# Optimization experiments

Hardware: AMD Instinct MI355X
Metric: run time of the kernel (lower is better)

Reference implementation:

```python
import jax, jax.numpy as jnp
import numpy as np

B, N, IN, LAT, HID = 64, 128, 5, 3, 64
ALPHA = 0.1
NEG_SLOPE = 0.2  # GATv2Conv default negative_slope


def _w(key, fan_in, shape):
    return jax.random.normal(key, shape, jnp.float32) * (1.0 / np.sqrt(fan_in))


def setup_inputs():
    key = jax.random.key(0)
    ks = iter(jax.random.split(key, 64))
    d = {}
    d["batch"] = jax.random.normal(next(ks), (B, N, IN), jnp.float32)
    d["enc_w1"] = _w(next(ks), IN, (IN, HID));   d["enc_b1"] = jnp.zeros((HID,), jnp.float32)
    d["enc_w2"] = _w(next(ks), HID, (HID, HID)); d["enc_b2"] = jnp.zeros((HID,), jnp.float32)
    d["enc_w3"] = _w(next(ks), HID, (HID, LAT)); d["enc_b3"] = jnp.zeros((LAT,), jnp.float32)
    for i, cin in zip((1, 2, 3, 4), (1, HID, HID, HID)):
        d[f"g{i}_wl"] = _w(next(ks), cin, (cin, HID)); d[f"g{i}_bl"] = jnp.zeros((HID,), jnp.float32)
        d[f"g{i}_wr"] = _w(next(ks), cin, (cin, HID)); d[f"g{i}_br"] = jnp.zeros((HID,), jnp.float32)
        d[f"g{i}_att"] = _w(next(ks), HID, (HID,));    d[f"g{i}_b"] = jnp.zeros((HID,), jnp.float32)
    d["lab_w"] = _w(next(ks), HID, (HID, 4)); d["lab_b"] = jnp.zeros((4,), jnp.float32)
    d["val_w"] = _w(next(ks), HID, (HID, 1)); d["val_b"] = jnp.zeros((1,), jnp.float32)
    d["skip_w"] = _w(next(ks), LAT, (LAT, HID)); d["skip_b"] = jnp.zeros((HID,), jnp.float32)
    return d


def _gabriel_adj(p):
    """Gabriel graph adjacency, p: [N, LAT] -> bool [N, N] (symmetric, no diag).
    Edge (i,j) survives iff no witness k with |p_k - mid_ij|^2 < |p_i - p_j|^2 / 4."""
    n = p.shape[0]
    mid = 0.5 * (p[:, None, :] + p[None, :, :])                      # [n,n,d]
    r2 = 0.25 * jnp.sum((p[:, None, :] - p[None, :, :]) ** 2, -1)    # [n,n]
    pk2 = jnp.sum(p * p, -1)                                         # [n]
    m2 = jnp.sum(mid * mid, -1)                                      # [n,n]
    # d2[k,i,j] = |p_k - mid_ij|^2 via expansion (avoids [n,n,n,d] tensor)
    d2 = pk2[:, None, None] - 2.0 * jnp.einsum('kd,ijd->kij', p, mid) + m2[None]
    idx = jnp.arange(n)
    not_ij = (idx[:, None, None] != idx[None, :, None]) & (idx[:, None, None] != idx[None, None, :])
    blocked = jnp.any((d2 < r2[None]) & not_ij, axis=0)              # [n,n]
    return (~blocked) & (idx[:, None] != idx[None, :])


def _gatv2(x, adj, wl, bl, wr, br, att, b):
    """Dense single-head GATv2 (PyG GATv2Conv semantics, self-loops already in adj).
    x: [B,N,Cin], adj: bool [B,N,N] (adj[b,i,j] => edge j->i)."""
    hl = x @ wl + bl   # source transform (lin_l)
    hr = x @ wr + br   # target transform (lin_r)
    e = jax.nn.leaky_relu(hr[:, :, None, :] + hl[:, None, :, :], NEG_SLOPE)  # [B,i,j,H]
    s = jnp.einsum('bijh,h->bij', e, att)
    s = jnp.where(adj, s, -1e30)
    a = jax.nn.softmax(s, axis=-1)                                   # softmax over neighbors j of i
    return jnp.einsum('bij,bjh->bih', a, hl) + b


def reference(batch, enc_w1, enc_b1, enc_w2, enc_b2, enc_w3, enc_b3,
              g1_wl, g1_bl, g1_wr, g1_br, g1_att, g1_b,
              g2_wl, g2_bl, g2_wr, g2_br, g2_att, g2_b,
              g3_wl, g3_bl, g3_wr, g3_br, g3_att, g3_b,
              g4_wl, g4_bl, g4_wr, g4_br, g4_att, g4_b,
              lab_w, lab_b, val_w, val_b, skip_w, skip_b):
    relu = jax.nn.relu
    h = relu(batch @ enc_w1 + enc_b1)
    h = relu(h @ enc_w2 + enc_b2)
    latent = h @ enc_w3 + enc_b3                                     # [B,N,3]

    adj = jax.vmap(_gabriel_adj)(jax.lax.stop_gradient(latent))      # bool [B,N,N]
    adj_sl = adj | jnp.eye(N, dtype=bool)                            # add_self_loops=True

    x0 = latent[..., 2:3]                                            # node feature = 3rd latent coord
    x1 = relu(_gatv2(x0, adj_sl, g1_wl, g1_bl, g1_wr, g1_br, g1_att, g1_b))
    x2 = relu(_gatv2(x1, adj_sl, g2_wl, g2_bl, g2_wr, g2_br, g2_att, g2_b))
    skip = latent @ skip_w + skip_b
    x3 = relu(_gatv2(x2, adj_sl, g3_wl, g3_bl, g3_wr, g3_br, g3_att, g3_b) + ALPHA * skip)
    logits = x3 @ lab_w + lab_b                                      # [B,N,4]
    x4 = relu(_gatv2(x2, adj_sl, g4_wl, g4_bl, g4_wr, g4_br, g4_att, g4_b) + ALPHA * skip)
    values = x4 @ val_w + val_b                                      # [B,N,1]

    # dense edge attributes: pairwise latent distances masked by the Gabriel adjacency
    d2p = jnp.sum((latent[:, :, None, :] - latent[:, None, :, :]) ** 2, -1)
    edge_dist = jnp.sqrt(jnp.where(adj, d2p, 1.0)) * adj

    return (batch[:, :, :4], batch[:, :, 4:5], logits, values, latent, adj, edge_dist)
```

## Files before the change

### kernel.cpp

```cpp
#include <hip/hip_runtime.h>

#define BB 64
#define NN 128
#define INF_ 5
#define LATD 3
#define HIDD 64

__device__ __forceinline__ float bflo(unsigned u) { return __uint_as_float(u << 16); }
__device__ __forceinline__ float bfhi(unsigned u) { return __uint_as_float(u & 0xffff0000u); }
__device__ __forceinline__ unsigned bfpack(float a, float b) {
    unsigned ua = __float_as_uint(a), ub = __float_as_uint(b);
    unsigned ra = (ua + 0x7fffu + ((ua >> 16) & 1u)) >> 16;
    unsigned rb = (ub + 0x7fffu + ((ub >> 16) & 1u)) >> 16;
    return ra | (rb << 16);
}

__global__ __launch_bounds__(256) void enc_kernel(
    const float* __restrict__ batch,
    const float* __restrict__ w1, const float* __restrict__ b1,
    const float* __restrict__ w2, const float* __restrict__ b2,
    const float* __restrict__ w3, const float* __restrict__ b3,
    double* __restrict__ aos,
    float* __restrict__ o0, float* __restrict__ o1, float* __restrict__ o4,
    float* __restrict__ o5)
{
    const int b = blockIdx.x;
    const int n0 = blockIdx.y * 32;
    const int tid = threadIdx.x;
    const int w = tid >> 6, lane = tid & 63;

    {
        const int blk = blockIdx.x * 4 + blockIdx.y;
        float4* z = (float4*)o5 + (size_t)blk * 2048;
        float4 zero = make_float4(0.f, 0.f, 0.f, 0.f);
        for (int q = tid; q < 2048; q += 256) z[q] = zero;
    }

    __shared__ double xs[32][6];
    __shared__ double w1s[INF_][HIDD];
    __shared__ float  w2s[HIDD * HIDD];
    __shared__ double w3s[HIDD][LATD];
    __shared__ double b1s[HIDD], b2s[HIDD], b3s[LATD];

    for (int idx = tid; idx < 32 * INF_; idx += 256) {
        int n = idx / INF_, c = idx % INF_;
        float v = batch[((size_t)b * NN + n0 + n) * INF_ + c];
        xs[n][c] = (double)v;
        if (c < 4) o0[((size_t)b * NN + n0 + n) * 4 + c] = v;
        else       o1[(size_t)b * NN + n0 + n] = v;
    }
    for (int idx = tid; idx < INF_ * HIDD; idx += 256)
        w1s[idx / HIDD][idx % HIDD] = (double)w1[idx];
    for (int idx = tid; idx < HIDD * HIDD; idx += 256)
        w2s[idx] = w2[idx];
    for (int idx = tid; idx < HIDD * LATD; idx += 256)
        w3s[idx / LATD][idx % LATD] = (double)w3[idx];
    if (tid < HIDD) {
        b1s[tid] = (double)b1[tid];
        b2s[tid] = (double)b2[tid];
    }
    if (tid < LATD) b3s[tid] = (double)b3[tid];
    __syncthreads();

    for (int r = 0; r < 8; ++r) {
        const int nl = w * 8 + r;
        const int n = n0 + nl;
        double h1v = b1s[lane];
        for (int k = 0; k < INF_; ++k) h1v += xs[nl][k] * w1s[k][lane];
        h1v = fmax(h1v, 0.0);
        double h2v = b2s[lane];
        for (int k = 0; k < HIDD; ++k) {
            double h1k = __shfl(h1v, k, 64);
            h2v += h1k * (double)w2s[k * HIDD + lane];
        }
        h2v = fmax(h2v, 0.0);
        double l0 = h2v * w3s[lane][0];
        double l1 = h2v * w3s[lane][1];
        double l2 = h2v * w3s[lane][2];
        for (int o = 32; o >= 1; o >>= 1) {
            l0 += __shfl_xor(l0, o, 64);
            l1 += __shfl_xor(l1, o, 64);
            l2 += __shfl_xor(l2, o, 64);
        }
        l0 += b3s[0]; l1 += b3s[1]; l2 += b3s[2];
        if (lane == 0) {
            double* A = aos + ((size_t)b * NN + n) * 4;
            A[0] = l0; A[1] = l1; A[2] = l2;
            A[3] = l0 * l0 + l1 * l1 + l2 * l2;
        }
        if (lane < LATD) {
            double lv = (lane == 0) ? l0 : ((lane == 1) ? l1 : l2);
            o4[((size_t)b * NN + n) * LATD + lane] = (float)lv;
        }
    }
}

__global__ __launch_bounds__(256) void gabriel_kernel(
    const double* __restrict__ aos,
    float* __restrict__ o5, float* __restrict__ o6)
{
    const int b = blockIdx.y;
    const int w = threadIdx.x >> 6, lane = threadIdx.x & 63;
    const int u = blockIdx.x * 4 + w;
    const int v = u >> 1, par = u & 1;

    __shared__ double4 Ps[NN];
    const double2* src = (const double2*)(aos + (size_t)b * NN * 4);
    double2* dst = (double2*)Ps;
    for (int idx = threadIdx.x; idx < NN * 2; idx += 256) dst[idx] = src[idx];
    __syncthreads();

    const double4 A  = Ps[lane];
    const double4 Bq = Ps[lane + 64];

    for (int half = 0; half < 2; ++half) {
        const int i = (half == 0) ? v : 126 - v;
        if (half == 1 && i == v) break;
        const int jstart = (half == 0) ? (v + 1) : (127 - v);
        const int j0 = jstart + ((jstart ^ par) & 1);
        const double4 pi = Ps[i];
        const double aix = A.x - pi.x,  aiy = A.y - pi.y,  aiz = A.z - pi.z;
        const double bix = Bq.x - pi.x, biy = Bq.y - pi.y, biz = Bq.z - pi.z;
        const bool mA = (lane != i), mB = (lane + 64 != i);
        for (int j = j0; j < NN; j += 2) {
            double4 pj = Ps[j];
            double ajx = A.x - pj.x,  ajy = A.y - pj.y,  ajz = A.z - pj.z;
            double bjx = Bq.x - pj.x, bjy = Bq.y - pj.y, bjz = Bq.z - pj.z;
            double dA = aix * ajx + aiy * ajy + aiz * ajz;
            double dB = bix * bjx + biy * bjy + biz * bjz;
            bool tA = (dA < 0.0) && mA && (lane != j);
            bool tB = (dB < 0.0) && mB && (lane + 64 != j);
            if (!__any(tA || tB)) {
                if (lane == 0) {
                    double dx = pi.x - pj.x, dy = pi.y - pj.y, dz = pi.z - pj.z;
                    float d = (float)sqrt(dx * dx + dy * dy + dz * dz);
                    size_t ij = ((size_t)b * NN + i) * NN + j;
                    size_t ji = ((size_t)b * NN + j) * NN + i;
                    o5[ij] = 1.0f; o5[ji] = 1.0f;
                    o6[ij] = d;    o6[ji] = d;
                }
            }
        }
    }
}

template <int CIN>
__device__ __forceinline__ void lin_body(
    int b, int n0, const float* __restrict__ xin, const float* __restrict__ latf,
    const float* __restrict__ wl, const float* __restrict__ bl,
    const float* __restrict__ wr, const float* __restrict__ br,
    unsigned* __restrict__ hlp, unsigned* __restrict__ hrp,
    float4* xs4, int tid)
{
    float* xsh = (float*)xs4;
    if constexpr (CIN == 64) {
        const float4* src = (const float4*)(xin + ((size_t)b * NN + n0) * HIDD);
        for (int idx = tid; idx < 32 * 16; idx += 256) xs4[idx] = src[idx];
    } else {
        if (tid < 32) xsh[tid] = latf[((size_t)b * NN + n0 + tid) * LATD + 2];
    }
    __syncthreads();

    const int w = tid >> 6, lane = tid & 63;
    float wc[CIN];
    #pragma unroll
    for (int k = 0; k < CIN; ++k) wc[k] = wl[k * HIDD + lane];
    float bv = bl[lane];
    for (int m = 0; m < 8; ++m) {
        int nl = w * 8 + m;
        float acc = bv;
        if constexpr (CIN == 64) {
            #pragma unroll
            for (int t = 0; t < 16; ++t) {
                float4 q = xs4[nl * 16 + t];
                acc = fmaf(q.x, wc[4 * t + 0], acc);
                acc = fmaf(q.y, wc[4 * t + 1], acc);
                acc = fmaf(q.z, wc[4 * t + 2], acc);
                acc = fmaf(q.w, wc[4 * t + 3], acc);
            }
        } else acc = fmaf(xsh[nl], wc[0], acc);
        float partner = __shfl_xor(acc, 1, 64);
        if ((lane & 1) == 0)
            hlp[((size_t)b * NN + n0 + nl) * 32 + (lane >> 1)] = bfpack(acc, partner);
    }
    #pragma unroll
    for (int k = 0; k < CIN; ++k) wc[k] = wr[k * HIDD + lane];
    bv = br[lane];
    for (int m = 0; m < 8; ++m) {
        int nl = w * 8 + m;
        float acc = bv;
        if constexpr (CIN == 64) {
            #pragma unroll
            for (int t = 0; t < 16; ++t) {
                float4 q = xs4[nl * 16 + t];
                acc = fmaf(q.x, wc[4 * t + 0], acc);
                acc = fmaf(q.y, wc[4 * t + 1], acc);
                acc = fmaf(q.z, wc[4 * t + 2], acc);
                acc = fmaf(q.w, wc[4 * t + 3], acc);
            }
        } else acc = fmaf(xsh[nl], wc[0], acc);
        float partner = __shfl_xor(acc, 1, 64);
        if ((lane & 1) == 0)
            hrp[((size_t)b * NN + n0 + nl) * 32 + (lane >> 1)] = bfpack(acc, partner);
    }
}

template <int CIN>
__global__ __launch_bounds__(256) void lin_kernel(
    const float* __restrict__ xin, const float* __restrict__ latf,
    const float* __restrict__ wl, const float* __restrict__ bl,
    const float* __restrict__ wr, const float* __restrict__ br,
    unsigned* __restrict__ hlp, unsigned* __restrict__ hrp)
{
    __shared__ float4 xs4[(CIN == 64) ? 32 * 16 : 8];
    lin_body<CIN>(blockIdx.x >> 2, (blockIdx.x & 3) << 5, xin, latf,
                  wl, bl, wr, br, hlp, hrp, xs4, threadIdx.x);
}

__global__ __launch_bounds__(256) void lin34_kernel(
    const float* __restrict__ xin,
    const float* __restrict__ wl3, const float* __restrict__ bl3,
    const float* __restrict__ wr3, const float* __restrict__ br3,
    const float* __restrict__ wl4, const float* __restrict__ bl4,
    const float* __restrict__ wr4, const float* __restrict__ br4,
    unsigned* __restrict__ hl3p, unsigned* __restrict__ hr3p,
    unsigned* __restrict__ hl4p, unsigned* __restrict__ hr4p)
{
    __shared__ float4 xs4[32 * 16];
    const int b = blockIdx.x >> 2, n0 = (blockIdx.x & 3) << 5;
    if (blockIdx.y == 0)
        lin_body<64>(b, n0, xin, nullptr, wl3, bl3, wr3, br3, hl3p, hr3p, xs4, threadIdx.x);
    else
        lin_body<64>(b, n0, xin, nullptr, wl4, bl4, wr4, br4, hl4p, hr4p, xs4, threadIdx.x);
}

struct AttnS {
    float  hls[NN * 66];
    float2 as2[4][NN];
    float2 hr2[8][32];
    float2 att2[32];
};

template <int C>
__device__ __forceinline__ void attn_v3(
    int b, int i0, int tid, AttnS& s,
    const unsigned* __restrict__ hlp, const unsigned* __restrict__ hrp,
    const float* __restrict__ att, const float* __restrict__ bias,
    const float* __restrict__ adjf, const float* __restrict__ latf,
    const float* __restrict__ skw, const float* __restrict__ skb,
    float* __restrict__ xout,
    const float* __restrict__ head_w, const float* __restrict__ head_b,
    float* __restrict__ head_out)
{
    const int w = tid >> 6, lane = tid & 63;

    {
        const unsigned* src = hlp + (size_t)b * NN * 32;
        for (int idx = tid; idx < NN * 32; idx += 256) {
            int j = idx >> 5, c = idx & 31;
            unsigned u = src[idx];
            *(float2*)&s.hls[j * 66 + 2 * c] = make_float2(bflo(u), bfhi(u));
        }
        unsigned u = hrp[((size_t)b * NN + i0) * 32 + tid];
        ((float2*)s.hr2)[tid] = make_float2(bflo(u), bfhi(u));
        if (tid < 32) s.att2[tid] = make_float2(att[2 * tid], att[2 * tid + 1]);
    }
    float bsv = bias[lane];
    float sw0 = 0.f, sw1 = 0.f, sw2 = 0.f, sbv = 0.f;
    if (skw != nullptr) {
        sw0 = skw[lane]; sw1 = skw[64 + lane]; sw2 = skw[128 + lane];
        sbv = skb[lane];
    }
    __syncthreads();

    const int il0 = w * 2, il1 = il0 + 1;
    const int i_0 = i0 + il0, i_1 = i0 + il1;

    float s00 = 0.f, s01 = 0.f, s10 = 0.f, s11 = 0.f;
    {
        const float* hl0 = &s.hls[lane * 66];
        const float* hl1 = &s.hls[(lane + 64) * 66];
        #pragma unroll
        for (int c = 0; c < 32; ++c) {
            float2 av = s.att2[c];
            float2 r0 = s.hr2[il0][c];
            float2 r1 = s.hr2[il1][c];
            float2 g0 = *(const float2*)&hl0[2 * c];
            float2 g1 = *(const float2*)&hl1[2 * c];
            float e;
            e = r0.x + g0.x; e = fmaxf(e, 0.2f * e); s00 = fmaf(av.x, e, s00);
            e = r0.y + g0.y; e = fmaxf(e, 0.2f * e); s00 = fmaf(av.y, e, s00);
            e = r0.x + g1.x; e = fmaxf(e, 0.2f * e); s01 = fmaf(av.x, e, s01);
            e = r0.y + g1.y; e = fmaxf(e, 0.2f * e); s01 = fmaf(av.y, e, s01);
            e = r1.x + g0.x; e = fmaxf(e, 0.2f * e); s10 = fmaf(av.x, e, s10);
            e = r1.y + g0.y; e = fmaxf(e, 0.2f * e); s10 = fmaf(av.y, e, s10);
            e = r1.x + g1.x; e = fmaxf(e, 0.2f * e); s11 = fmaf(av.x, e, s11);
            e = r1.y + g1.y; e = fmaxf(e, 0.2f * e); s11 = fmaf(av.y, e, s11);
        }
    }
    {
        const float* ar0 = adjf + ((size_t)b * NN + i_0) * NN;
        const float* ar1 = adjf + ((size_t)b * NN + i_1) * NN;
        if (!((ar0[lane] != 0.f)      || (lane == i_0)))      s00 = -1e30f;
        if (!((ar0[lane + 64] != 0.f) || (lane + 64 == i_0))) s01 = -1e30f;
        if (!((ar1[lane] != 0.f)      || (lane == i_1)))      s10 = -1e30f;
        if (!((ar1[lane + 64] != 0.f) || (lane + 64 == i_1))) s11 = -1e30f;
    }
    float m0 = fmaxf(s00, s01), m1 = fmaxf(s10, s11);
    for (int o = 32; o >= 1; o >>= 1) {
        m0 = fmaxf(m0, __shfl_xor(m0, o, 64));
        m1 = fmaxf(m1, __shfl_xor(m1, o, 64));
    }
    float e00 = __expf(s00 - m0), e01 = __expf(s01 - m0);
    float e10 = __expf(s10 - m1), e11 = __expf(s11 - m1);
    float z0 = e00 + e01, z1 = e10 + e11;
    for (int o = 32; o >= 1; o >>= 1) {
        z0 += __shfl_xor(z0, o, 64);
        z1 += __shfl_xor(z1, o, 64);
    }
    float iv0 = 1.f / z0, iv1 = 1.f / z1;
    s.as2[w][lane]      = make_float2(e00 * iv0, e10 * iv1);
    s.as2[w][lane + 64] = make_float2(e01 * iv0, e11 * iv1);

    float o0a = 0.f, o1a = 0.f;
    for (int j = 0; j < NN; ++j) {
        float2 av = s.as2[w][j];
        float hv = s.hls[j * 66 + lane];
        o0a = fmaf(av.x, hv, o0a);
        o1a = fmaf(av.y, hv, o1a);
    }

    #pragma unroll
    for (int r = 0; r < 2; ++r) {
        const int i = (r == 0) ? i_0 : i_1;
        float out = ((r == 0) ? o0a : o1a) + bsv;
        if (skw != nullptr) {
            const float* lr = latf + ((size_t)b * NN + i) * LATD;
            float sk = sbv;
            sk = fmaf(lr[0], sw0, sk);
            sk = fmaf(lr[1], sw1, sk);
            sk = fmaf(lr[2], sw2, sk);
            out += 0.1f * sk;
        }
        out = fmaxf(out, 0.f);
        if constexpr (C == 0) {
            xout[((size_t)b * NN + i) * HIDD + lane] = out;
        } else {
            float hv[C > 0 ? C : 1];
            #pragma unroll
            for (int c = 0; c < C; ++c) {
                float vv = out * head_w[lane * C + c];
                for (int o = 32; o >= 1; o >>= 1) vv += __shfl_xor(vv, o, 64);
                hv[c] = vv + head_b[c];
            }
            if (lane == 0)
                for (int c = 0; c < C; ++c)
                    head_out[((size_t)b * NN + i) * C + c] = hv[c];
        }
    }
}

__global__ __launch_bounds__(256, 4) void attn12_kernel(
    const unsigned* __restrict__ hlp, const unsigned* __restrict__ hrp,
    const float* __restrict__ att, const float* __restrict__ bias,
    const float* __restrict__ adjf, float* __restrict__ xout)
{
    __shared__ AttnS s;
    attn_v3<0>(blockIdx.x >> 4, (blockIdx.x & 15) << 3, threadIdx.x, s,
               hlp, hrp, att, bias, adjf, nullptr, nullptr, nullptr,
               xout, nullptr, nullptr, nullptr);
}

__global__ __launch_bounds__(256, 4) void attn34_kernel(
    const unsigned* __restrict__ hl3p, const unsigned* __restrict__ hr3p,
    const unsigned* __restrict__ hl4p, const unsigned* __restrict__ hr4p,
    const float* __restrict__ att3, const float* __restrict__ b3,
    const float* __restrict__ att4, const float* __restrict__ b4,
    const float* __restrict__ adjf, const float* __restrict__ latf,
    const float* __restrict__ skw, const float* __restrict__ skb,
    const float* __restrict__ lab_w, const float* __restrict__ lab_b, float* __restrict__ o2,
    const float* __restrict__ val_w, const float* __restrict__ val_b, float* __restrict__ o3)
{
    __shared__ AttnS s;
    const int b = blockIdx.x >> 4, i0 = (blockIdx.x & 15) << 3;
    if (blockIdx.y == 0)
        attn_v3<4>(b, i0, threadIdx.x, s, hl3p, hr3p, att3, b3, adjf, latf,
                   skw, skb, nullptr, lab_w, lab_b, o2);
    else
        attn_v3<1>(b, i0, threadIdx.x, s, hl4p, hr4p, att4, b4, adjf, latf,
                   skw, skb, nullptr, val_w, val_b, o3);
}

extern "C" void kernel_launch(void* const* d_in, const int* in_sizes, int n_in,
                              void* d_out, int out_size, void* d_ws, size_t ws_size,
                              hipStream_t stream)
{
    const float* batch  = (const float*)d_in[0];
    const float* enc_w1 = (const float*)d_in[1];
    const float* enc_b1 = (const float*)d_in[2];
    const float* enc_w2 = (const float*)d_in[3];
    const float* enc_b2 = (const float*)d_in[4];
    const float* enc_w3 = (const float*)d_in[5];
    const float* enc_b3 = (const float*)d_in[6];
    const float* g_wl[4]  = {(const float*)d_in[7],  (const float*)d_in[13], (const float*)d_in[19], (const float*)d_in[25]};
    const float* g_bl[4]  = {(const float*)d_in[8],  (const float*)d_in[14], (const float*)d_in[20], (const float*)d_in[26]};
    const float* g_wr[4]  = {(const float*)d_in[9],  (const float*)d_in[15], (const float*)d_in[21], (const float*)d_in[27]};
    const float* g_br[4]  = {(const float*)d_in[10], (const float*)d_in[16], (const float*)d_in[22], (const float*)d_in[28]};
    const float* g_att[4] = {(const float*)d_in[11], (const float*)d_in[17], (const float*)d_in[23], (const float*)d_in[29]};
    const float* g_b[4]   = {(const float*)d_in[12], (const float*)d_in[18], (const float*)d_in[24], (const float*)d_in[30]};
    const float* lab_w = (const float*)d_in[31];
    const float* lab_b = (const float*)d_in[32];
    const float* val_w = (const float*)d_in[33];
    const float* val_b = (const float*)d_in[34];
    const float* skw   = (const float*)d_in[35];
    const float* skb   = (const float*)d_in[36];

    float* out = (float*)d_out;
    float* o0 = out;
    float* o1 = out + 32768;
    float* o2 = out + 40960;
    float* o3 = out + 73728;
    float* o4 = out + 81920;
    float* o5 = out + 106496;
    float* o6 = out + 1155072;

    char* p = (char*)d_ws;
    auto carve = [&](size_t bytes) { void* r = (void*)p; p += (bytes + 255) & ~(size_t)255; return r; };
    double*   aos  = (double*)  carve((size_t)BB * NN * 4 * 8);
    float*    xA   = (float*)   carve((size_t)BB * NN * HIDD * 4);
    float*    xB   = (float*)   carve((size_t)BB * NN * HIDD * 4);
    unsigned* hlp  = (unsigned*)carve((size_t)BB * NN * 32 * 4);
    unsigned* hrp  = (unsigned*)carve((size_t)BB * NN * 32 * 4);
    unsigned* hl3p = (unsigned*)carve((size_t)BB * NN * 32 * 4);
    unsigned* hr3p = (unsigned*)carve((size_t)BB * NN * 32 * 4);

    enc_kernel<<<dim3(BB, 4), 256, 0, stream>>>(batch, enc_w1, enc_b1, enc_w2, enc_b2,
                                                enc_w3, enc_b3, aos, o0, o1, o4, o5);
    gabriel_kernel<<<dim3(32, BB), 256, 0, stream>>>(aos, o5, o6);

    lin_kernel<1><<<BB * 4, 256, 0, stream>>>(nullptr, o4, g_wl[0], g_bl[0], g_wr[0], g_br[0], hlp, hrp);
    attn12_kernel<<<BB * 16, 256, 0, stream>>>(hlp, hrp, g_att[0], g_b[0], o5, xA);
    lin_kernel<64><<<BB * 4, 256, 0, stream>>>(xA, nullptr, g_wl[1], g_bl[1], g_wr[1], g_br[1], hlp, hrp);
    attn12_kernel<<<BB * 16, 256, 0, stream>>>(hlp, hrp, g_att[1], g_b[1], o5, xB);
    lin34_kernel<<<dim3(BB * 4, 2), 256, 0, stream>>>(xB,
        g_wl[2], g_bl[2], g_wr[2], g_br[2], g_wl[3], g_bl[3], g_wr[3], g_br[3],
        hl3p, hr3p, hlp, hrp);
    attn34_kernel<<<dim3(BB * 16, 2), 256, 0, stream>>>(hl3p, hr3p, hlp, hrp,
        g_att[2], g_b[2], g_att[3], g_b[3], o5, o4, skw, skb,
        lab_w, lab_b, o2, val_w, val_b, o3);
}
```

Before: 304.9 us.

## Fuse GATv2 linear projections into preceding attention kernels

Removes the separate lin kernels by computing the next layer's left/right projections at the end of each attention block, using the aggregated per-node outputs held in registers plus weight matrices staged in shared memory. Layer 1's rank-1 projection is computed inline at the start of the first attention kernel. This cuts three kernel launches and the fp32 xA/xB activation round trips through global memory. In exchange, every attention block reloads the full 64x64 weight matrices into LDS (four times in attnB), adds extra barriers, and performs a serial 64-step shuffle matvec.

```diff
diff --git a/kernel.cpp b/kernel.cpp
--- a/kernel.cpp
+++ b/kernel.cpp
@@ -144,96 +144,6 @@
     }
 }
 
-template <int CIN>
-__device__ __forceinline__ void lin_body(
-    int b, int n0, const float* __restrict__ xin, const float* __restrict__ latf,
-    const float* __restrict__ wl, const float* __restrict__ bl,
-    const float* __restrict__ wr, const float* __restrict__ br,
-    unsigned* __restrict__ hlp, unsigned* __restrict__ hrp,
-    float4* xs4, int tid)
-{
-    float* xsh = (float*)xs4;
-    if constexpr (CIN == 64) {
-        const float4* src = (const float4*)(xin + ((size_t)b * NN + n0) * HIDD);
-        for (int idx = tid; idx < 32 * 16; idx += 256) xs4[idx] = src[idx];
-    } else {
-        if (tid < 32) xsh[tid] = latf[((size_t)b * NN + n0 + tid) * LATD + 2];
-    }
-    __syncthreads();
-
-    const int w = tid >> 6, lane = tid & 63;
-    float wc[CIN];
-    #pragma unroll
-    for (int k = 0; k < CIN; ++k) wc[k] = wl[k * HIDD + lane];
-    float bv = bl[lane];
-    for (int m = 0; m < 8; ++m) {
-        int nl = w * 8 + m;
-        float acc = bv;
-        if constexpr (CIN == 64) {
-            #pragma unroll
-            for (int t = 0; t < 16; ++t) {
-                float4 q = xs4[nl * 16 + t];
-                acc = fmaf(q.x, wc[4 * t + 0], acc);
-                acc = fmaf(q.y, wc[4 * t + 1], acc);
-                acc = fmaf(q.z, wc[4 * t + 2], acc);
-                acc = fmaf(q.w, wc[4 * t + 3], acc);
-            }
-        } else acc = fmaf(xsh[nl], wc[0], acc);
-        float partner = __shfl_xor(acc, 1, 64);
-        if ((lane & 1) == 0)
-            hlp[((size_t)b * NN + n0 + nl) * 32 + (lane >> 1)] = bfpack(acc, partner);
-    }
-    #pragma unroll
-    for (int k = 0; k < CIN; ++k) wc[k] = wr[k * HIDD + lane];
-    bv = br[lane];
-    for (int m = 0; m < 8; ++m) {
-        int nl = w * 8 + m;
-        float acc = bv;
-        if constexpr (CIN == 64) {
-            #pragma unroll
-            for (int t = 0; t < 16; ++t) {
-                float4 q = xs4[nl * 16 + t];
-                acc = fmaf(q.x, wc[4 * t + 0], acc);
-                acc = fmaf(q.y, wc[4 * t + 1], acc);
-                acc = fmaf(q.z, wc[4 * t + 2], acc);
-                acc = fmaf(q.w, wc[4 * t + 3], acc);
-            }
-        } else acc = fmaf(xsh[nl], wc[0], acc);
-        float partner = __shfl_xor(acc, 1, 64);
-        if ((lane & 1) == 0)
-            hrp[((size_t)b * NN + n0 + nl) * 32 + (lane >> 1)] = bfpack(acc, partner);
-    }
-}
-
-template <int CIN>
-__global__ __launch_bounds__(256) void lin_kernel(
-    const float* __restrict__ xin, const float* __restrict__ latf,
-    const float* __restrict__ wl, const float* __restrict__ bl,
-    const float* __restrict__ wr, const float* __restrict__ br,
-    unsigned* __restrict__ hlp, unsigned* __restrict__ hrp)
-{
-    __shared__ float4 xs4[(CIN == 64) ? 32 * 16 : 8];
-    lin_body<CIN>(blockIdx.x >> 2, (blockIdx.x & 3) << 5, xin, latf,
-                  wl, bl, wr, br, hlp, hrp, xs4, threadIdx.x);
-}
-
-__global__ __launch_bounds__(256) void lin34_kernel(
-    const float* __restrict__ xin,
-    const float* __restrict__ wl3, const float* __restrict__ bl3,
-    const float* __restrict__ wr3, const float* __restrict__ br3,
-    const float* __restrict__ wl4, const float* __restrict__ bl4,
-    const float* __restrict__ wr4, const float* __restrict__ br4,
-    unsigned* __restrict__ hl3p, unsigned* __restrict__ hr3p,
-    unsigned* __restrict__ hl4p, unsigned* __restrict__ hr4p)
-{
-    __shared__ float4 xs4[32 * 16];
-    const int b = blockIdx.x >> 2, n0 = (blockIdx.x & 3) << 5;
-    if (blockIdx.y == 0)
-        lin_body<64>(b, n0, xin, nullptr, wl3, bl3, wr3, br3, hl3p, hr3p, xs4, threadIdx.x);
-    else
-        lin_body<64>(b, n0, xin, nullptr, wl4, bl4, wr4, br4, hl4p, hr4p, xs4, threadIdx.x);
-}
-
 struct AttnS {
     float  hls[NN * 66];
     float2 as2[4][NN];
@@ -241,41 +151,28 @@
     float2 att2[32];
 };
 
-template <int C>
-__device__ __forceinline__ void attn_v3(
-    int b, int i0, int tid, AttnS& s,
+__device__ __forceinline__ void attn_stage_packed(
+    AttnS& s, int tid, int b, int i0,
     const unsigned* __restrict__ hlp, const unsigned* __restrict__ hrp,
-    const float* __restrict__ att, const float* __restrict__ bias,
-    const float* __restrict__ adjf, const float* __restrict__ latf,
-    const float* __restrict__ skw, const float* __restrict__ skb,
-    float* __restrict__ xout,
-    const float* __restrict__ head_w, const float* __restrict__ head_b,
-    float* __restrict__ head_out)
-{
-    const int w = tid >> 6, lane = tid & 63;
-
-    {
-        const unsigned* src = hlp + (size_t)b * NN * 32;
-        for (int idx = tid; idx < NN * 32; idx += 256) {
-            int j = idx >> 5, c = idx & 31;
-            unsigned u = src[idx];
-            *(float2*)&s.hls[j * 66 + 2 * c] = make_float2(bflo(u), bfhi(u));
-        }
-        unsigned u = hrp[((size_t)b * NN + i0) * 32 + tid];
-        ((float2*)s.hr2)[tid] = make_float2(bflo(u), bfhi(u));
-        if (tid < 32) s.att2[tid] = make_float2(att[2 * tid], att[2 * tid + 1]);
-    }
-    float bsv = bias[lane];
-    float sw0 = 0.f, sw1 = 0.f, sw2 = 0.f, sbv = 0.f;
-    if (skw != nullptr) {
-        sw0 = skw[lane]; sw1 = skw[64 + lane]; sw2 = skw[128 + lane];
-        sbv = skb[lane];
-    }
-    __syncthreads();
-
+    const float* __restrict__ att)
+{
+    const unsigned* src = hlp + (size_t)b * NN * 32;
+    for (int idx = tid; idx < NN * 32; idx += 256) {
+        int j = idx >> 5, c = idx & 31;
+        unsigned u = src[idx];
+        *(float2*)&s.hls[j * 66 + 2 * c] = make_float2(bflo(u), bfhi(u));
+    }
+    unsigned u = hrp[((size_t)b * NN + i0) * 32 + tid];
+    ((float2*)s.hr2)[tid] = make_float2(bflo(u), bfhi(u));
+    if (tid < 32) s.att2[tid] = make_float2(att[2 * tid], att[2 * tid + 1]);
+}
+
+__device__ __forceinline__ void attn_phase(
+    AttnS& s, int b, int i0, int w, int lane,
+    const float* __restrict__ adjf, float& agg0, float& agg1)
+{
     const int il0 = w * 2, il1 = il0 + 1;
     const int i_0 = i0 + il0, i_1 = i0 + il1;
-
     float s00 = 0.f, s01 = 0.f, s10 = 0.f, s11 = 0.f;
     {
         const float* hl0 = &s.hls[lane * 66];
@@ -321,7 +218,6 @@
     float iv0 = 1.f / z0, iv1 = 1.f / z1;
     s.as2[w][lane]      = make_float2(e00 * iv0, e10 * iv1);
     s.as2[w][lane + 64] = make_float2(e01 * iv0, e11 * iv1);
-
     float o0a = 0.f, o1a = 0.f;
     for (int j = 0; j < NN; ++j) {
         float2 av = s.as2[w][j];
@@ -329,49 +225,148 @@
         o0a = fmaf(av.x, hv, o0a);
         o1a = fmaf(av.y, hv, o1a);
     }
+    agg0 = o0a; agg1 = o1a;
+}
+
+__device__ __forceinline__ void matvec_store(
+    AttnS& s, int tid, int w, int lane, float out0, float out1,
+    int b, int i0, const float* __restrict__ wmat, const float* __restrict__ bvec,
+    unsigned* __restrict__ outp)
+{
+    __syncthreads();
+    for (int idx = tid; idx < HIDD * HIDD; idx += 256) s.hls[idx] = wmat[idx];
+    __syncthreads();
+    float acc0 = bvec[lane], acc1 = acc0;
+    for (int h = 0; h < HIDD; ++h) {
+        float wv = s.hls[h * HIDD + lane];
+        acc0 = fmaf(__shfl(out0, h, 64), wv, acc0);
+        acc1 = fmaf(__shfl(out1, h, 64), wv, acc1);
+    }
+    float p0 = __shfl_xor(acc0, 1, 64);
+    float p1 = __shfl_xor(acc1, 1, 64);
+    if ((lane & 1) == 0) {
+        outp[((size_t)b * NN + i0 + w * 2 + 0) * 32 + (lane >> 1)] = bfpack(acc0, p0);
+        outp[((size_t)b * NN + i0 + w * 2 + 1) * 32 + (lane >> 1)] = bfpack(acc1, p1);
+    }
+}
+
+__global__ __launch_bounds__(256, 4) void attnA_kernel(
+    const float* __restrict__ latf,
+    const float* __restrict__ wl1, const float* __restrict__ bl1,
+    const float* __restrict__ wr1, const float* __restrict__ br1,
+    const float* __restrict__ att, const float* __restrict__ bias,
+    const float* __restrict__ adjf,
+    const float* __restrict__ wl2, const float* __restrict__ bl2,
+    const float* __restrict__ wr2, const float* __restrict__ br2,
+    unsigned* __restrict__ hl2p, unsigned* __restrict__ hr2p)
+{
+    __shared__ AttnS s;
+    const int bx = blockIdx.x;
+    const int b = bx >> 4, i0 = (bx & 15) << 3;
+    const int tid = threadIdx.x, w = tid >> 6, lane = tid & 63;
+
+    {
+        float wv = wl1[lane], bv = bl1[lane];
+        for (int m = 0; m < 32; ++m) {
+            int j = w + 4 * m;
+            float x0 = latf[((size_t)b * NN + j) * LATD + 2];
+            s.hls[j * 66 + lane] = fmaf(x0, wv, bv);
+        }
+    }
+    {
+        int il = tid >> 5, c = tid & 31;
+        float x0 = latf[((size_t)b * NN + i0 + il) * LATD + 2];
+        s.hr2[il][c] = make_float2(fmaf(x0, wr1[2 * c], br1[2 * c]),
+                                   fmaf(x0, wr1[2 * c + 1], br1[2 * c + 1]));
+    }
+    if (tid < 32) s.att2[tid] = make_float2(att[2 * tid], att[2 * tid + 1]);
+    float bsv = bias[lane];
+    __syncthreads();
+
+    float agg0, agg1;
+    attn_phase(s, b, i0, w, lane, adjf, agg0, agg1);
+    float out0 = fmaxf(agg0 + bsv, 0.f);
+    float out1 = fmaxf(agg1 + bsv, 0.f);
+
+    matvec_store(s, tid, w, lane, out0, out1, b, i0, wl2, bl2, hl2p);
+    matvec_store(s, tid, w, lane, out0, out1, b, i0, wr2, br2, hr2p);
+}
+
+__global__ __launch_bounds__(256, 4) void attnB_kernel(
+    const unsigned* __restrict__ hlp, const unsigned* __restrict__ hrp,
+    const float* __restrict__ att, const float* __restrict__ bias,
+    const float* __restrict__ adjf,
+    const float* __restrict__ wl3, const float* __restrict__ bl3,
+    const float* __restrict__ wr3, const float* __restrict__ br3,
+    const float* __restrict__ wl4, const float* __restrict__ bl4,
+    const float* __restrict__ wr4, const float* __restrict__ br4,
+    unsigned* __restrict__ hl3p, unsigned* __restrict__ hr3p,
+    unsigned* __restrict__ hl4p, unsigned* __restrict__ hr4p)
+{
+    __shared__ AttnS s;
+    const int bx = blockIdx.x;
+    const int b = bx >> 4, i0 = (bx & 15) << 3;
+    const int tid = threadIdx.x, w = tid >> 6, lane = tid & 63;
+
+    attn_stage_packed(s, tid, b, i0, hlp, hrp, att);
+    float bsv = bias[lane];
+    __syncthreads();
+
+    float agg0, agg1;
+    attn_phase(s, b, i0, w, lane, adjf, agg0, agg1);
+    float out0 = fmaxf(agg0 + bsv, 0.f);
+    float out1 = fmaxf(agg1 + bsv, 0.f);
+
+    matvec_store(s, tid, w, lane, out0, out1, b, i0, wl3, bl3, hl3p);
+    matvec_store(s, tid, w, lane, out0, out1, b, i0, wr3, br3, hr3p);
+    matvec_store(s, tid, w, lane, out0, out1, b, i0, wl4, bl4, hl4p);
+    matvec_store(s, tid, w, lane, out0, out1, b, i0, wr4, br4, hr4p);
+}
+
+template <int C>
+__device__ __forceinline__ void attn_head(
+    AttnS& s, int tid, int b, int i0,
+    const unsigned* __restrict__ hlp, const unsigned* __restrict__ hrp,
+    const float* __restrict__ att, const float* __restrict__ bias,
+    const float* __restrict__ adjf, const float* __restrict__ latf,
+    const float* __restrict__ skw, const float* __restrict__ skb,
+    const float* __restrict__ head_w, const float* __restrict__ head_b,
+    float* __restrict__ head_out)
+{
+    const int w = tid >> 6, lane = tid & 63;
+    attn_stage_packed(s, tid, b, i0, hlp, hrp, att);
+    float bsv = bias[lane];
+    float sw0 = skw[lane], sw1 = skw[64 + lane], sw2 = skw[128 + lane];
+    float sbv = skb[lane];
+    __syncthreads();
+
+    float agg0, agg1;
+    attn_phase(s, b, i0, w, lane, adjf, agg0, agg1);
 
     #pragma unroll
     for (int r = 0; r < 2; ++r) {
-        const int i = (r == 0) ? i_0 : i_1;
-        float out = ((r == 0) ? o0a : o1a) + bsv;
-        if (skw != nullptr) {
-            const float* lr = latf + ((size_t)b * NN + i) * LATD;
-            float sk = sbv;
-            sk = fmaf(lr[0], sw0, sk);
-            sk = fmaf(lr[1], sw1, sk);
-            sk = fmaf(lr[2], sw2, sk);
-            out += 0.1f * sk;
-        }
-        out = fmaxf(out, 0.f);
-        if constexpr (C == 0) {
-            xout[((size_t)b * NN + i) * HIDD + lane] = out;
-        } else {
-            float hv[C > 0 ? C : 1];
-            #pragma unroll
-            for (int c = 0; c < C; ++c) {
-                float vv = out * head_w[lane * C + c];
-                for (int o = 32; o >= 1; o >>= 1) vv += __shfl_xor(vv, o, 64);
-                hv[c] = vv + head_b[c];
-            }
-            if (lane == 0)
-                for (int c = 0; c < C; ++c)
-                    head_out[((size_t)b * NN + i) * C + c] = hv[c];
-        }
-    }
-}
-
-__global__ __launch_bounds__(256, 4) void attn12_kernel(
-    const unsigned* __restrict__ hlp, const unsigned* __restrict__ hrp,
-    const float* __restrict__ att, const float* __restrict__ bias,
-    const float* __restrict__ adjf, float* __restrict__ xout)
-{
-    __shared__ AttnS s;
-    attn_v3<0>(blockIdx.x >> 4, (blockIdx.x & 15) << 3, threadIdx.x, s,
-               hlp, hrp, att, bias, adjf, nullptr, nullptr, nullptr,
-               xout, nullptr, nullptr, nullptr);
-}
-
-__global__ __launch_bounds__(256, 4) void attn34_kernel(
+        const int i = i0 + w * 2 + r;
+        float out = ((r == 0) ? agg0 : agg1) + bsv;
+        const float* lr = latf + ((size_t)b * NN + i) * LATD;
+        float sk = sbv;
+        sk = fmaf(lr[0], sw0, sk);
+        sk = fmaf(lr[1], sw1, sk);
+        sk = fmaf(lr[2], sw2, sk);
+        out = fmaxf(out + 0.1f * sk, 0.f);
+        float hv[C];
+        #pragma unroll
+        for (int c = 0; c < C; ++c) {
+            float vv = out * head_w[lane * C + c];
+            for (int o = 32; o >= 1; o >>= 1) vv += __shfl_xor(vv, o, 64);
+            hv[c] = vv + head_b[c];
+        }
+        if (lane == 0)
+            for (int c = 0; c < C; ++c)
+                head_out[((size_t)b * NN + i) * C + c] = hv[c];
+    }
+}
+
+__global__ __launch_bounds__(256, 4) void attnCD_kernel(
     const unsigned* __restrict__ hl3p, const unsigned* __restrict__ hr3p,
     const unsigned* __restrict__ hl4p, const unsigned* __restrict__ hr4p,
     const float* __restrict__ att3, const float* __restrict__ b3,
@@ -384,11 +379,11 @@
     __shared__ AttnS s;
     const int b = blockIdx.x >> 4, i0 = (blockIdx.x & 15) << 3;
     if (blockIdx.y == 0)
-        attn_v3<4>(b, i0, threadIdx.x, s, hl3p, hr3p, att3, b3, adjf, latf,
-                   skw, skb, nullptr, lab_w, lab_b, o2);
+        attn_head<4>(s, threadIdx.x, b, i0, hl3p, hr3p, att3, b3, adjf, latf,
+                     skw, skb, lab_w, lab_b, o2);
     else
-        attn_v3<1>(b, i0, threadIdx.x, s, hl4p, hr4p, att4, b4, adjf, latf,
-                   skw, skb, nullptr, val_w, val_b, o3);
+        attn_head<1>(s, threadIdx.x, b, i0, hl4p, hr4p, att4, b4, adjf, latf,
+                     skw, skb, val_w, val_b, o3);
 }
 
 extern "C" void kernel_launch(void* const* d_in, const int* in_sizes, int n_in,
@@ -427,25 +422,26 @@
     char* p = (char*)d_ws;
     auto carve = [&](size_t bytes) { void* r = (void*)p; p += (bytes + 255) & ~(size_t)255; return r; };
     double*   aos  = (double*)  carve((size_t)BB * NN * 4 * 8);
-    float*    xA   = (float*)   carve((size_t)BB * NN * HIDD * 4);
-    float*    xB   = (float*)   carve((size_t)BB * NN * HIDD * 4);
-    unsigned* hlp  = (unsigned*)carve((size_t)BB * NN * 32 * 4);
-    unsigned* hrp  = (unsigned*)carve((size_t)BB * NN * 32 * 4);
+    unsigned* hl2p = (unsigned*)carve((size_t)BB * NN * 32 * 4);
+    unsigned* hr2p = (unsigned*)carve((size_t)BB * NN * 32 * 4);
     unsigned* hl3p = (unsigned*)carve((size_t)BB * NN * 32 * 4);
     unsigned* hr3p = (unsigned*)carve((size_t)BB * NN * 32 * 4);
+    unsigned* hl4p = (unsigned*)carve((size_t)BB * NN * 32 * 4);
+    unsigned* hr4p = (unsigned*)carve((size_t)BB * NN * 32 * 4);
 
     enc_kernel<<<dim3(BB, 4), 256, 0, stream>>>(batch, enc_w1, enc_b1, enc_w2, enc_b2,
                                                 enc_w3, enc_b3, aos, o0, o1, o4, o5);
     gabriel_kernel<<<dim3(32, BB), 256, 0, stream>>>(aos, o5, o6);
 
-    lin_kernel<1><<<BB * 4, 256, 0, stream>>>(nullptr, o4, g_wl[0], g_bl[0], g_wr[0], g_br[0], hlp, hrp);
-    attn12_kernel<<<BB * 16, 256, 0, stream>>>(hlp, hrp, g_att[0], g_b[0], o5, xA);
-    lin_kernel<64><<<BB * 4, 256, 0, stream>>>(xA, nullptr, g_wl[1], g_bl[1], g_wr[1], g_br[1], hlp, hrp);
-    attn12_kernel<<<BB * 16, 256, 0, stream>>>(hlp, hrp, g_att[1], g_b[1], o5, xB);
-    lin34_kernel<<<dim3(BB * 4, 2), 256, 0, stream>>>(xB,
-        g_wl[2], g_bl[2], g_wr[2], g_br[2], g_wl[3], g_bl[3], g_wr[3], g_br[3],
-        hl3p, hr3p, hlp, hrp);
-    attn34_kernel<<<dim3(BB * 16, 2), 256, 0, stream>>>(hl3p, hr3p, hlp, hrp,
+    attnA_kernel<<<BB * 16, 256, 0, stream>>>(o4,
+        g_wl[0], g_bl[0], g_wr[0], g_br[0], g_att[0], g_b[0], o5,
+        g_wl[1], g_bl[1], g_wr[1], g_br[1], hl2p, hr2p);
+    attnB_kernel<<<BB * 16, 256, 0, stream>>>(hl2p, hr2p,
+        g_att[1], g_b[1], o5,
+        g_wl[2], g_bl[2], g_wr[2], g_br[2],
+        g_wl[3], g_bl[3], g_wr[3], g_br[3],
+        hl3p, hr3p, hl4p, hr4p);
+    attnCD_kernel<<<dim3(BB * 16, 2), 256, 0, stream>>>(hl3p, hr3p, hl4p, hr4p,
         g_att[2], g_b[2], g_att[3], g_b[3], o5, o4, skw, skb,
         lab_w, lab_b, o2, val_w, val_b, o3);
 }
```

Result: faster. 298.3 us (-2.1%).
